# Kernel tuning notes

Measured on AMD Instinct MI355X. Metric: run time of the kernel, lower is better.

Reference implementation:

```python
import jax, jax.numpy as jnp
import numpy as np

ALPHA = 0.2        # LeakyReLU negative slope
NEG_INF = -9.0e15  # mask value used by the torch code


def _gat_layer(x, adj_mask, W, a, concat):
    """Dense multi-head GAT layer.
    x: (N, in_f); adj_mask: (N, N) bool; W: (H, in_f, F); a: (H, 2F, 1).
    Math identical to torch: a_input[p,q] = [h[q], h[p]] so
    e[p,q] = leakyrelu(h[q]@a1 + h[p]@a2) with a = [a1; a2].
    """
    F_out = W.shape[-1]
    h = jnp.einsum('nf,hfo->hno', x, W)                  # (H, N, F)
    a1 = a[:, :F_out, 0]                                 # (H, F) -> applied to h_i (column index q)
    a2 = a[:, F_out:, 0]                                 # (H, F) -> applied to h_j (row index p)
    s1 = jnp.einsum('hnf,hf->hn', h, a1)                 # (H, N)
    s2 = jnp.einsum('hnf,hf->hn', h, a2)                 # (H, N)
    e = jax.nn.leaky_relu(s1[:, None, :] + s2[:, :, None], ALPHA)  # (H, N, N), e[h,p,q]
    e = jnp.where(adj_mask[None, :, :], e, NEG_INF)
    att = jax.nn.softmax(e, axis=-1)                     # softmax over q (dim=1 in torch)
    h_prime = jnp.einsum('hpq,hqf->hpf', att, h)         # (H, N, F)
    if concat:
        N = x.shape[0]
        return h_prime.transpose(1, 0, 2).reshape(N, -1)  # head-order concat, (N, H*F)
    return h_prime.mean(axis=0)                           # (N, F)


def setup_inputs() -> dict:
    key = jax.random.key(0)
    ks = jax.random.split(key, 16)
    N, IN, HID, OUT, H = 2048, 10, 64, 3, 4

    def w(k, shape, fan_in):
        return (jax.random.normal(k, shape, dtype=jnp.float32) * (1.0 / np.sqrt(fan_in))).astype(jnp.float32)

    return {
        'node_features': jax.random.normal(ks[0], (N, IN), dtype=jnp.float32),
        'adj_matrix': jax.random.randint(ks[1], (N, N), 0, 2).astype(jnp.int32),
        'enc_W1': w(ks[2], (IN, HID), IN), 'enc_b1': jnp.zeros((HID,), jnp.float32),
        'enc_W2': w(ks[3], (HID, HID), HID), 'enc_b2': jnp.zeros((HID,), jnp.float32),
        'gat_W0': w(ks[4], (H, HID, HID), HID), 'gat_a0': w(ks[5], (H, 2 * HID, 1), 2 * HID),
        'gat_W1': w(ks[6], (H, HID * H, HID), HID * H), 'gat_a1': w(ks[7], (H, 2 * HID, 1), 2 * HID),
        'gat_W2': w(ks[8], (H, HID * H, OUT), HID * H), 'gat_a2': w(ks[9], (H, 2 * OUT, 1), 2 * OUT),
        'cls_W1': w(ks[10], (OUT, 32), OUT), 'cls_b1': jnp.zeros((32,), jnp.float32),
        'cls_W2': w(ks[11], (32, 1), 32), 'cls_b2': jnp.zeros((1,), jnp.float32),
    }


def reference(node_features, adj_matrix, enc_W1, enc_b1, enc_W2, enc_b2,
              gat_W0, gat_a0, gat_W1, gat_a1, gat_W2, gat_a2,
              cls_W1, cls_b1, cls_W2, cls_b2):
    adj = adj_matrix > 0
    # feature encoder (dropout = identity in eval)
    x = jax.nn.relu(node_features @ enc_W1 + enc_b1) @ enc_W2 + enc_b2
    # GAT stack with ELU between layers
    x = jax.nn.elu(_gat_layer(x, adj, gat_W0, gat_a0, concat=True))
    x = jax.nn.elu(_gat_layer(x, adj, gat_W1, gat_a1, concat=True))
    emb = jax.nn.elu(_gat_layer(x, adj, gat_W2, gat_a2, concat=False))  # (N, OUT)
    # edge classifier: |emb[q] - emb[p]| -> MLP -> sigmoid, (N, N)
    diff = jnp.abs(emb[None, :, :] - emb[:, None, :])                   # (N, N, OUT)
    hidden = jax.nn.relu(diff @ cls_W1 + cls_b1)                        # (N, N, 32)
    edge_probs = jax.nn.sigmoid((hidden @ cls_W2 + cls_b2)[..., 0])     # (N, N)
    return emb, edge_probs
```

## Files before the change

kernel.cpp:

```cpp
#include <hip/hip_runtime.h>
#include <hip/hip_bf16.h>
#include <hip/hip_fp16.h>

#define ALPHA 0.2f
#define LOG2E 1.44269504088896340736f
constexpr int N = 2048;
constexpr int NW = N / 64;

typedef __attribute__((ext_vector_type(8))) short short8v;
typedef __attribute__((ext_vector_type(4))) float f32x4;

__device__ inline unsigned short bf16_rne(float f) {
  unsigned u = __float_as_uint(f);
  return (unsigned short)((u + 0x7fffu + ((u >> 16) & 1u)) >> 16);
}

__device__ inline __half2 relu_h2(__half2 a) {
  unsigned ua = *(unsigned*)&a, ur;
  asm("v_pk_max_f16 %0, %1, 0" : "=v"(ur) : "v"(ua));
  return *(__half2*)&ur;
}


__global__ void __launch_bounds__(512) prep_kernel(
    const float* __restrict__ nf, const int* __restrict__ adj,
    const float* __restrict__ encW1, const float* __restrict__ encb1,
    const float* __restrict__ encW2, const float* __restrict__ encb2,
    const float* __restrict__ gatW0, const float* __restrict__ gatW1,
    unsigned long long* __restrict__ mask,
    unsigned short* __restrict__ wt0hi, unsigned short* __restrict__ wt0lo,
    unsigned short* __restrict__ wt1hi, unsigned short* __restrict__ wt1lo,
    unsigned short* __restrict__ x0hi) {
  const int t = threadIdx.x, b = blockIdx.x;
  {
    int gwave = b * 8 + (t >> 6), lane = t & 63;
#pragma unroll
    for (int i = 0; i < 16; i++) {
      int word = gwave * 16 + i;
      unsigned long long m = __ballot(adj[(size_t)word * 64 + lane] != 0);
      if (lane == 0) mask[word] = m;
    }
  }
  {
    int gtid = b * 512 + t;
    if (gtid < 16384) {
      int head = gtid >> 12, idx = gtid & 4095;
      int o = idx >> 6, k = idx & 63;
      float v = gatW0[(head * 64 + k) * 64 + o];
      unsigned short hb = bf16_rne(v);
      size_t oi = (((((size_t)head * 4 + (o >> 4)) * 2 + (k >> 5)) * 4 + ((k & 31) >> 3)) * 16 + (o & 15)) * 8 + (k & 7);
      wt0hi[oi] = hb;
      wt0lo[oi] = bf16_rne(v - __uint_as_float((unsigned)hb << 16));
    }
    if (gtid < 65536) {
      int head = gtid >> 14, idx = gtid & 16383;
      int o = idx >> 8, k = idx & 255;
      float v = gatW1[((size_t)head * 256 + k) * 64 + o];
      unsigned short hb = bf16_rne(v);
      size_t oi = (((((size_t)head * 4 + (o >> 4)) * 8 + (k >> 5)) * 4 + ((k & 31) >> 3)) * 16 + (o & 15)) * 8 + (k & 7);
      wt1hi[oi] = hb;
      wt1lo[oi] = bf16_rne(v - __uint_as_float((unsigned)hb << 16));
    }
  }
  if (b < 256) {
    __shared__ float nfs[2][4][10], x1e[2][4][64], pred[2][4][4][64];
    const int half = t >> 8, tl = t & 255;
    const int j = tl >> 6, o = tl & 63;
    const int n0 = b * 8 + half * 4;
    if (tl < 40) nfs[half][tl / 10][tl % 10] = nf[n0 * 10 + tl];
    __syncthreads();
    float acc = encb1[o];
#pragma unroll
    for (int k = 0; k < 10; k++) acc = fmaf(nfs[half][j][k], encW1[k * 64 + o], acc);
    x1e[half][j][o] = fmaxf(acc, 0.f);
    __syncthreads();
    {
      const int kq = j;
      float pp0 = 0, pp1 = 0, pp2 = 0, pp3 = 0;
#pragma unroll
      for (int kk = 0; kk < 16; kk++) {
        int k = kq * 16 + kk;
        float wv = encW2[k * 64 + o];
        pp0 = fmaf(x1e[half][0][k], wv, pp0);
        pp1 = fmaf(x1e[half][1][k], wv, pp1);
        pp2 = fmaf(x1e[half][2][k], wv, pp2);
        pp3 = fmaf(x1e[half][3][k], wv, pp3);
      }
      pred[half][kq][0][o] = pp0; pred[half][kq][1][o] = pp1;
      pred[half][kq][2][o] = pp2; pred[half][kq][3][o] = pp3;
    }
    __syncthreads();
    float v = encb2[o] + pred[half][0][j][o] + pred[half][1][j][o] +
              pred[half][2][j][o] + pred[half][3][j][o];
    const int n = n0 + j;
    size_t oi = ((((size_t)(n >> 4) * 2 + (o >> 5)) * 4 + ((o & 31) >> 3)) * 16 + (n & 15)) * 8 + (o & 7);
    x0hi[oi] = bf16_rne(v);
  }
}

template <int K>
__global__ void __launch_bounds__(256, 4)
proj_mfma_kernel(const unsigned short* __restrict__ xhi,
                 const unsigned short* __restrict__ wthi, const unsigned short* __restrict__ wtlo,
                 const float* __restrict__ avec,
                 unsigned short* __restrict__ hT, float* __restrict__ s1, float* __restrict__ s2,
                 float* __restrict__ pm1) {
  constexpr int KS = K / 32;
  const int head = blockIdx.y;
  const int n0 = blockIdx.x * 16;
  const int wave = threadIdx.x >> 6, lane = threadIdx.x & 63;
  const int il = lane & 15, kgrp = lane >> 4;
  const int o0 = wave * 16;
  const unsigned short* __restrict__ Ah = wthi + ((size_t)(head * 4 + wave) * KS) * 512 + lane * 8;
  const unsigned short* __restrict__ Al = wtlo + ((size_t)(head * 4 + wave) * KS) * 512 + lane * 8;
  const unsigned short* __restrict__ Bh = xhi + ((size_t)blockIdx.x * KS) * 512 + lane * 8;
  f32x4 acc = {0, 0, 0, 0};
#pragma unroll
  for (int ks = 0; ks < KS; ks++) {
    short8v ah = *(const short8v*)(Ah + ks * 512);
    short8v al = *(const short8v*)(Al + ks * 512);
    short8v bh = *(const short8v*)(Bh + ks * 512);
    acc = __builtin_amdgcn_mfma_f32_16x16x32_bf16(ah, bh, acc, 0, 0, 0);
    acc = __builtin_amdgcn_mfma_f32_16x16x32_bf16(al, bh, acc, 0, 0, 0);
  }
  const int n = n0 + il;
  const size_t cbase = (((size_t)head * (N / 32) + (n >> 5)) * 4 + wave) * 512;
  const int sub = ((n & 31) >> 3) * 16;
  const int eoff = n & 7;
  float p1 = 0.f, p2 = 0.f;
#pragma unroll
  for (int r = 0; r < 4; r++) {
    const int o = o0 + kgrp * 4 + r;
    hT[cbase + (size_t)(sub + kgrp * 4 + r) * 8 + eoff] = bf16_rne(acc[r]);
    p1 = fmaf(acc[r], avec[head * 128 + o], p1);
    p2 = fmaf(acc[r], avec[head * 128 + 64 + o], p2);
  }
  p1 += __shfl_xor(p1, 16); p1 += __shfl_xor(p1, 32);
  p2 += __shfl_xor(p2, 16); p2 += __shfl_xor(p2, 32);
  __shared__ float s1p[4][16], s2p[4][16];
  if (kgrp == 0) { s1p[wave][il] = p1; s2p[wave][il] = p2; }
  __syncthreads();
  if (threadIdx.x < 16) {
    int nn = n0 + threadIdx.x;
    float v1 = (s1p[0][threadIdx.x] + s1p[1][threadIdx.x] + s1p[2][threadIdx.x] + s1p[3][threadIdx.x]) * LOG2E;
    float v2 = (s2p[0][threadIdx.x] + s2p[1][threadIdx.x] + s2p[2][threadIdx.x] + s2p[3][threadIdx.x]) * LOG2E;
    s1[head * N + nn] = v1;
    s2[head * N + nn] = v2;
    float m1 = v1;
#pragma unroll
    for (int s = 1; s < 16; s <<= 1) m1 = fmaxf(m1, __shfl_xor(m1, s));
    if (threadIdx.x == 0) pm1[head * 128 + blockIdx.x] = m1;
  }
}

template <bool WF32, bool WBF>
__global__ void __launch_bounds__(512, 4)
agg_fused_kernel(const unsigned short* __restrict__ hTu,
                 const float* __restrict__ s1, const float* __restrict__ s2,
                 const float* __restrict__ pm1,
                 const unsigned long long* __restrict__ mask,
                 float* __restrict__ xout, unsigned short* __restrict__ xohi) {
  const int head = blockIdx.y;
  const int p0 = blockIdx.x * 16;
  const int wave = threadIdx.x >> 6, lane = threadIdx.x & 63;
  const int col = lane & 15, kgrp = lane >> 4;
  const int p = p0 + col;
  const float s2pv = s2[head * N + p];
  float sm = fmaxf(pm1[head * 128 + lane], pm1[head * 128 + 64 + lane]);
#pragma unroll
  for (int s = 1; s < 64; s <<= 1) sm = fmaxf(sm, __shfl_xor(sm, s));
  const float mraw = sm + s2pv;
  const float mp = fmaxf(mraw, ALPHA * mraw);
  const float c1 = s2pv - mp;
  const float c2 = ALPHA * s2pv - mp;
  const float* __restrict__ s1h = s1 + head * N;
  const int qbase = wave * 256;
  const unsigned long long* __restrict__ mr = mask + (size_t)p * NW + (qbase >> 6);
  unsigned long long mw0 = mr[0], mw1 = mr[1], mw2 = mr[2], mw3 = mr[3];
  const unsigned short* __restrict__ bbase =
      hTu + (((size_t)head * (N / 32) + wave * 8) * 4) * 512 + lane * 8;

  f32x4 acc[4] = {{0,0,0,0},{0,0,0,0},{0,0,0,0},{0,0,0,0}};
  float wsum = 0.f;
#pragma unroll
  for (int ks = 0; ks < 8; ks++) {
    const int qa = qbase + ks * 32 + kgrp * 8;
    float4 s1v0 = *(const float4*)(s1h + qa);
    float4 s1v1 = *(const float4*)(s1h + qa + 4);
    unsigned long long mwsel = (ks < 2) ? mw0 : (ks < 4) ? mw1 : (ks < 6) ? mw2 : mw3;
    unsigned b8 = (unsigned)((mwsel >> ((ks & 1) * 32 + kgrp * 8)) & 0xFFull);
    float sv[8] = {s1v0.x, s1v0.y, s1v0.z, s1v0.w, s1v1.x, s1v1.y, s1v1.z, s1v1.w};
    float w[8];
#pragma unroll
    for (int e = 0; e < 8; e++) {
      float lr = fmaxf(sv[e] + c1, fmaf(sv[e], ALPHA, c2));
      float ww = exp2f(lr);
      ww = ((b8 >> e) & 1u) ? ww : 0.f;
      wsum += ww;
      w[e] = ww;
    }
    union { short8v s; unsigned u[4]; } av;
#pragma unroll
    for (int e2 = 0; e2 < 4; e2++)
      asm("v_cvt_pk_bf16_f32 %0, %1, %2" : "=v"(av.u[e2]) : "v"(w[2 * e2]), "v"(w[2 * e2 + 1]));
#pragma unroll
    for (int ff = 0; ff < 4; ff++) {
      short8v b_hi = *(const short8v*)(bbase + ((size_t)ks * 4 + ff) * 512);
      acc[ff] = __builtin_amdgcn_mfma_f32_16x16x32_bf16(av.s, b_hi, acc[ff], 0, 0, 0);
    }
  }
  wsum += __shfl_xor(wsum, 16);
  wsum += __shfl_xor(wsum, 32);

  __shared__ float red[8][16][65];
  __shared__ float wred[8][16];
#pragma unroll
  for (int ff = 0; ff < 4; ff++)
#pragma unroll
    for (int r = 0; r < 4; r++)
      red[wave][kgrp * 4 + r][ff * 16 + col] = acc[ff][r];
  if (lane < 16) wred[wave][lane] = wsum;
  __syncthreads();
#pragma unroll
  for (int rep = 0; rep < 2; rep++) {
    int idx = threadIdx.x + rep * 512;
    int pl = idx >> 6, f = idx & 63;
    float num = 0.f, dn = 0.f;
#pragma unroll
    for (int w8 = 0; w8 < 8; w8++) { num += red[w8][pl][f]; dn += wred[w8][pl]; }
    float v = num / dn;
    v = v > 0.f ? v : (__expf(v) - 1.f);
    if (WF32) xout[(size_t)(p0 + pl) * 256 + head * 64 + f] = v;
    if (WBF) {
      size_t oi = ((((size_t)blockIdx.x * 8 + head * 2 + (f >> 5)) * 4 + ((f & 31) >> 3)) * 16 + pl) * 8 + (f & 7);
      xohi[oi] = bf16_rne(v);
    }
  }
}

__global__ void h3_kernel(const float* __restrict__ x, const float* __restrict__ W,
                          const float* __restrict__ a, float* __restrict__ h2,
                          float* __restrict__ s1, float* __restrict__ s2,
                          float* __restrict__ pm1h3) {
  const int n0 = blockIdx.x * 4;
  const int head = threadIdx.x >> 6, o = threadIdx.x & 63;
  __shared__ float xr[4][256];
  for (int k = threadIdx.x; k < 1024; k += 256) xr[k >> 8][k & 255] = x[(size_t)n0 * 256 + k];
  __syncthreads();
  const float* __restrict__ Wh = W + (size_t)head * 256 * 3;
  float m1 = -3.4e38f;
#pragma unroll
  for (int jj = 0; jj < 4; jj++) {
    float a0 = 0.f, a1 = 0.f, a2 = 0.f;
#pragma unroll
    for (int i = 0; i < 4; i++) {
      int k = o + 64 * i;
      float xv = xr[jj][k];
      a0 = fmaf(xv, Wh[k * 3 + 0], a0);
      a1 = fmaf(xv, Wh[k * 3 + 1], a1);
      a2 = fmaf(xv, Wh[k * 3 + 2], a2);
    }
    for (int s = 32; s; s >>= 1) {
      a0 += __shfl_xor(a0, s); a1 += __shfl_xor(a1, s); a2 += __shfl_xor(a2, s);
    }
    float p1 = (a0 * a[head * 6 + 0] + a1 * a[head * 6 + 1] + a2 * a[head * 6 + 2]) * LOG2E;
    float p2 = (a0 * a[head * 6 + 3] + a1 * a[head * 6 + 4] + a2 * a[head * 6 + 5]) * LOG2E;
    m1 = fmaxf(m1, p1);
    if (o == 0) {
      float* hq = h2 + ((size_t)head * N + n0 + jj) * 4;
      hq[0] = a0; hq[1] = a1; hq[2] = a2; hq[3] = 0.f;
      s1[head * N + n0 + jj] = p1;
      s2[head * N + n0 + jj] = p2;
    }
  }
  if (o == 0) pm1h3[head * 512 + blockIdx.x] = m1;
}

__global__ void agg2_kernel(const float* __restrict__ h2, const float* __restrict__ s1,
                            const float* __restrict__ s2, const float* __restrict__ pm1h3,
                            const unsigned long long* __restrict__ mask,
                            float* __restrict__ emb) {
  const int p = blockIdx.x;
  const int head = threadIdx.x >> 6, lane = threadIdx.x & 63;
  const float s2pv = s2[head * N + p];
  float sm = -3.4e38f;
  for (int i = lane; i < 512; i += 64) sm = fmaxf(sm, pm1h3[head * 512 + i]);
#pragma unroll
  for (int s = 1; s < 64; s <<= 1) sm = fmaxf(sm, __shfl_xor(sm, s));
  float mraw = sm + s2pv;
  const float mhv = fmaxf(mraw, ALPHA * mraw);
  const float c1 = s2pv - mhv;
  const float c2 = ALPHA * s2pv - mhv;
  const float* __restrict__ s1h = s1 + head * N;
  float a0 = 0.f, a1 = 0.f, a2 = 0.f, wsum = 0.f;
#pragma unroll 2
  for (int i = 0; i < 32; i++) {
    unsigned long long mwd = mask[(size_t)p * NW + i];
    int q = i * 64 + lane;
    if ((mwd >> lane) & 1ull) {
      float sv = s1h[q];
      float lr = fmaxf(sv + c1, fmaf(sv, ALPHA, c2));
      float w = exp2f(lr);
      float4 hv = *(const float4*)(h2 + ((size_t)head * N + q) * 4);
      a0 = fmaf(w, hv.x, a0);
      a1 = fmaf(w, hv.y, a1);
      a2 = fmaf(w, hv.z, a2);
      wsum += w;
    }
  }
  for (int s = 32; s; s >>= 1) {
    a0 += __shfl_xor(a0, s); a1 += __shfl_xor(a1, s);
    a2 += __shfl_xor(a2, s); wsum += __shfl_xor(wsum, s);
  }
  __shared__ float red[4][4];
  if (lane == 0) { red[head][0] = a0; red[head][1] = a1; red[head][2] = a2; red[head][3] = wsum; }
  __syncthreads();
  if (threadIdx.x < 3) {
    int f = threadIdx.x;
    float v = 0.f;
#pragma unroll
    for (int hh = 0; hh < 4; hh++) v += red[hh][f] / red[hh][3];
    v *= 0.25f;
    v = v > 0.f ? v : (__expf(v) - 1.f);
    emb[p * 3 + f] = v;
  }
}

__global__ void cls_kernel(const float* __restrict__ emb,
                           const float* __restrict__ W1, const float* __restrict__ b1,
                           const float* __restrict__ W2, const float* __restrict__ b2,
                           float* __restrict__ out) {
  int q = blockIdx.x * 256 + threadIdx.x;
  int p0 = blockIdx.y * 8;
  __shared__ float ep[8][3];
  __shared__ __half2 w1h[96], b1h[32], w2h[32];
  __shared__ float b2s;
  int t = threadIdx.x;
  if (t < 96) w1h[t] = __float2half2_rn(W1[t]);
  else if (t < 128) b1h[t - 96] = __float2half2_rn(b1[t - 96]);
  else if (t < 160) w2h[t - 128] = __float2half2_rn(W2[t - 128]);
  else if (t == 160) b2s = b2[0];
  else if (t >= 192 && t < 216) ((float*)ep)[t - 192] = emb[p0 * 3 + t - 192];
  __syncthreads();
  float e0 = emb[q * 3 + 0], e1 = emb[q * 3 + 1], e2 = emb[q * 3 + 2];
  __half2 d0[4], d1[4], d2[4];
#pragma unroll
  for (int ip = 0; ip < 4; ip++) {
    d0[ip] = __floats2half2_rn(fabsf(ep[2 * ip][0] - e0), fabsf(ep[2 * ip + 1][0] - e0));
    d1[ip] = __floats2half2_rn(fabsf(ep[2 * ip][1] - e1), fabsf(ep[2 * ip + 1][1] - e1));
    d2[ip] = __floats2half2_rn(fabsf(ep[2 * ip][2] - e2), fabsf(ep[2 * ip + 1][2] - e2));
  }
  const __half2 hz = __float2half2_rn(0.f);
  __half2 acc[4] = {hz, hz, hz, hz};
#pragma unroll
  for (int j = 0; j < 32; j++) {
    __half2 c0 = w1h[j], c1 = w1h[32 + j], c2 = w1h[64 + j], bb = b1h[j], w2 = w2h[j];
#pragma unroll
    for (int ip = 0; ip < 4; ip++) {
      __half2 hv = __hfma2(d0[ip], c0, __hfma2(d1[ip], c1, __hfma2(d2[ip], c2, bb)));
      hv = relu_h2(hv);
      acc[ip] = __hfma2(hv, w2, acc[ip]);
    }
  }
#pragma unroll
  for (int ip = 0; ip < 4; ip++) {
    float x0 = __low2float(acc[ip]) + b2s;
    float x1 = __high2float(acc[ip]) + b2s;
    out[(size_t)(p0 + 2 * ip) * N + q] = 1.f / (1.f + __expf(-x0));
    out[(size_t)(p0 + 2 * ip + 1) * N + q] = 1.f / (1.f + __expf(-x1));
  }
}

extern "C" void kernel_launch(void* const* d_in, const int* in_sizes, int n_in,
                              void* d_out, int out_size, void* d_ws, size_t ws_size,
                              hipStream_t stream) {
  const float* nf    = (const float*)d_in[0];
  const int*   adj   = (const int*)d_in[1];
  const float* encW1 = (const float*)d_in[2];
  const float* encb1 = (const float*)d_in[3];
  const float* encW2 = (const float*)d_in[4];
  const float* encb2 = (const float*)d_in[5];
  const float* gatW0 = (const float*)d_in[6];
  const float* gata0 = (const float*)d_in[7];
  const float* gatW1 = (const float*)d_in[8];
  const float* gata1 = (const float*)d_in[9];
  const float* gatW2 = (const float*)d_in[10];
  const float* gata2 = (const float*)d_in[11];
  const float* clsW1 = (const float*)d_in[12];
  const float* clsb1 = (const float*)d_in[13];
  const float* clsW2 = (const float*)d_in[14];
  const float* clsb2 = (const float*)d_in[15];

  float* ws = (float*)d_ws;
  unsigned short* hT   = (unsigned short*)ws;
  float* s1   = ws + 262144;
  float* s2   = s1 + 8192;
  float* pm1  = s2 + 8192;
  float* pm1h3= pm1 + 512;
  unsigned short* x0hi = (unsigned short*)(pm1h3 + 2048);
  unsigned short* wt0hi= x0hi + 131072;
  unsigned short* wt0lo= wt0hi + 16384;
  unsigned short* wt1hi= wt0lo + 16384;
  unsigned short* wt1lo= wt1hi + 65536;
  unsigned short* xAhi = wt1lo + 65536;
  float* xB   = (float*)(xAhi + 524288);
  float* h2   = xB + 524288;
  unsigned long long* mask = (unsigned long long*)(h2 + 32768);

  float* emb = (float*)d_out;
  float* eprob = emb + N * 3;

  prep_kernel<<<dim3(512), dim3(512), 0, stream>>>(
      nf, adj, encW1, encb1, encW2, encb2, gatW0, gatW1,
      mask, wt0hi, wt0lo, wt1hi, wt1lo, x0hi);

  proj_mfma_kernel<64><<<dim3(N / 16, 4), dim3(256), 0, stream>>>(
      x0hi, wt0hi, wt0lo, gata0, hT, s1, s2, pm1);
  agg_fused_kernel<false, true><<<dim3(N / 16, 4), dim3(512), 0, stream>>>(
      hT, s1, s2, pm1, mask, nullptr, xAhi);

  proj_mfma_kernel<256><<<dim3(N / 16, 4), dim3(256), 0, stream>>>(
      xAhi, wt1hi, wt1lo, gata1, hT, s1, s2, pm1);
  agg_fused_kernel<true, false><<<dim3(N / 16, 4), dim3(512), 0, stream>>>(
      hT, s1, s2, pm1, mask, xB, nullptr);

  h3_kernel<<<dim3(N / 4), dim3(256), 0, stream>>>(xB, gatW2, gata2, h2, s1, s2, pm1h3);
  agg2_kernel<<<dim3(N), dim3(256), 0, stream>>>(h2, s1, s2, pm1h3, mask, emb);

  cls_kernel<<<dim3(8, N / 8), dim3(256), 0, stream>>>(emb, clsW1, clsb1, clsW2, clsb2, eprob);
}
```

Baseline: 84.88 us.

## Fuse feature encoder and layer-0 weight conversion into first projection kernel

Moves the encoder MLP and the gatW0 bf16 hi/lo split out of prep_kernel into a new proj0_fused_kernel. That kernel computes the encoder output for its 16 nodes in shared memory and runs the layer-0 MFMA projection directly, so the x0hi and wt0 intermediate buffers are no longer written to and read back from global memory. In exchange, each of the 512 blocks recomputes the encoder for its nodes across all 4 heads and converts weights to bf16 on the fly. It also uses large shared arrays and several __syncthreads inside the loop, which can lower occupancy.

```diff
diff --git a/kernel.cpp b/kernel.cpp
--- a/kernel.cpp
+++ b/kernel.cpp
@@ -23,14 +23,9 @@
 
 
 __global__ void __launch_bounds__(512) prep_kernel(
-    const float* __restrict__ nf, const int* __restrict__ adj,
-    const float* __restrict__ encW1, const float* __restrict__ encb1,
-    const float* __restrict__ encW2, const float* __restrict__ encb2,
-    const float* __restrict__ gatW0, const float* __restrict__ gatW1,
+    const int* __restrict__ adj, const float* __restrict__ gatW1,
     unsigned long long* __restrict__ mask,
-    unsigned short* __restrict__ wt0hi, unsigned short* __restrict__ wt0lo,
-    unsigned short* __restrict__ wt1hi, unsigned short* __restrict__ wt1lo,
-    unsigned short* __restrict__ x0hi) {
+    unsigned short* __restrict__ wt1hi, unsigned short* __restrict__ wt1lo) {
   const int t = threadIdx.x, b = blockIdx.x;
   {
     int gwave = b * 8 + (t >> 6), lane = t & 63;
@@ -43,15 +38,6 @@
   }
   {
     int gtid = b * 512 + t;
-    if (gtid < 16384) {
-      int head = gtid >> 12, idx = gtid & 4095;
-      int o = idx >> 6, k = idx & 63;
-      float v = gatW0[(head * 64 + k) * 64 + o];
-      unsigned short hb = bf16_rne(v);
-      size_t oi = (((((size_t)head * 4 + (o >> 4)) * 2 + (k >> 5)) * 4 + ((k & 31) >> 3)) * 16 + (o & 15)) * 8 + (k & 7);
-      wt0hi[oi] = hb;
-      wt0lo[oi] = bf16_rne(v - __uint_as_float((unsigned)hb << 16));
-    }
     if (gtid < 65536) {
       int head = gtid >> 14, idx = gtid & 16383;
       int o = idx >> 8, k = idx & 255;
@@ -62,17 +48,34 @@
       wt1lo[oi] = bf16_rne(v - __uint_as_float((unsigned)hb << 16));
     }
   }
-  if (b < 256) {
-    __shared__ float nfs[2][4][10], x1e[2][4][64], pred[2][4][4][64];
-    const int half = t >> 8, tl = t & 255;
-    const int j = tl >> 6, o = tl & 63;
-    const int n0 = b * 8 + half * 4;
-    if (tl < 40) nfs[half][tl / 10][tl % 10] = nf[n0 * 10 + tl];
-    __syncthreads();
+}
+
+__global__ void __launch_bounds__(256, 4)
+proj0_fused_kernel(const float* __restrict__ nf,
+                   const float* __restrict__ encW1, const float* __restrict__ encb1,
+                   const float* __restrict__ encW2, const float* __restrict__ encb2,
+                   const float* __restrict__ gatW0, const float* __restrict__ avec,
+                   unsigned short* __restrict__ hT, float* __restrict__ s1, float* __restrict__ s2,
+                   float* __restrict__ pm1) {
+  const int head = blockIdx.y;
+  const int n0 = blockIdx.x * 16;
+  const int t = threadIdx.x;
+  __shared__ float nfs[16][10];
+  __shared__ float x1s[4][65];
+  __shared__ float preds[4][4][64];
+  __shared__ float xs[16][65];
+  __shared__ float ws0[64][65];
+  for (int idx = t; idx < 4096; idx += 256) {
+    ws0[idx >> 6][idx & 63] = gatW0[(size_t)head * 4096 + idx];
+  }
+  if (t < 160) nfs[t / 10][t % 10] = nf[(size_t)n0 * 10 + t];
+  __syncthreads();
+  const int j = t >> 6, o = t & 63;
+  for (int batch = 0; batch < 4; batch++) {
     float acc = encb1[o];
 #pragma unroll
-    for (int k = 0; k < 10; k++) acc = fmaf(nfs[half][j][k], encW1[k * 64 + o], acc);
-    x1e[half][j][o] = fmaxf(acc, 0.f);
+    for (int k = 0; k < 10; k++) acc = fmaf(nfs[batch * 4 + j][k], encW1[k * 64 + o], acc);
+    x1s[j][o] = fmaxf(acc, 0.f);
     __syncthreads();
     {
       const int kq = j;
@@ -81,31 +84,75 @@
       for (int kk = 0; kk < 16; kk++) {
         int k = kq * 16 + kk;
         float wv = encW2[k * 64 + o];
-        pp0 = fmaf(x1e[half][0][k], wv, pp0);
-        pp1 = fmaf(x1e[half][1][k], wv, pp1);
-        pp2 = fmaf(x1e[half][2][k], wv, pp2);
-        pp3 = fmaf(x1e[half][3][k], wv, pp3);
+        pp0 = fmaf(x1s[0][k], wv, pp0);
+        pp1 = fmaf(x1s[1][k], wv, pp1);
+        pp2 = fmaf(x1s[2][k], wv, pp2);
+        pp3 = fmaf(x1s[3][k], wv, pp3);
       }
-      pred[half][kq][0][o] = pp0; pred[half][kq][1][o] = pp1;
-      pred[half][kq][2][o] = pp2; pred[half][kq][3][o] = pp3;
+      preds[kq][0][o] = pp0; preds[kq][1][o] = pp1;
+      preds[kq][2][o] = pp2; preds[kq][3][o] = pp3;
     }
     __syncthreads();
-    float v = encb2[o] + pred[half][0][j][o] + pred[half][1][j][o] +
-              pred[half][2][j][o] + pred[half][3][j][o];
-    const int n = n0 + j;
-    size_t oi = ((((size_t)(n >> 4) * 2 + (o >> 5)) * 4 + ((o & 31) >> 3)) * 16 + (n & 15)) * 8 + (o & 7);
-    x0hi[oi] = bf16_rne(v);
-  }
-}
-
-template <int K>
+    xs[batch * 4 + j][o] = encb2[o] + preds[0][j][o] + preds[1][j][o] +
+                           preds[2][j][o] + preds[3][j][o];
+    __syncthreads();
+  }
+  const int wave = t >> 6, lane = t & 63;
+  const int il = lane & 15, kgrp = lane >> 4;
+  const int o0 = wave * 16;
+  f32x4 acc = {0, 0, 0, 0};
+#pragma unroll
+  for (int ks = 0; ks < 2; ks++) {
+    const int kbase = ks * 32 + kgrp * 8;
+    short8v ah, al, bh;
+#pragma unroll
+    for (int e = 0; e < 8; e++) {
+      float wv = ws0[kbase + e][o0 + il];
+      unsigned short hb = bf16_rne(wv);
+      ah[e] = (short)hb;
+      al[e] = (short)bf16_rne(wv - __uint_as_float((unsigned)hb << 16));
+      bh[e] = (short)bf16_rne(xs[il][kbase + e]);
+    }
+    acc = __builtin_amdgcn_mfma_f32_16x16x32_bf16(ah, bh, acc, 0, 0, 0);
+    acc = __builtin_amdgcn_mfma_f32_16x16x32_bf16(al, bh, acc, 0, 0, 0);
+  }
+  const int n = n0 + il;
+  const size_t cbase = (((size_t)head * (N / 32) + (n >> 5)) * 4 + wave) * 512;
+  const int sub = ((n & 31) >> 3) * 16;
+  const int eoff = n & 7;
+  float p1 = 0.f, p2 = 0.f;
+#pragma unroll
+  for (int r = 0; r < 4; r++) {
+    const int oo = o0 + kgrp * 4 + r;
+    hT[cbase + (size_t)(sub + kgrp * 4 + r) * 8 + eoff] = bf16_rne(acc[r]);
+    p1 = fmaf(acc[r], avec[head * 128 + oo], p1);
+    p2 = fmaf(acc[r], avec[head * 128 + 64 + oo], p2);
+  }
+  p1 += __shfl_xor(p1, 16); p1 += __shfl_xor(p1, 32);
+  p2 += __shfl_xor(p2, 16); p2 += __shfl_xor(p2, 32);
+  __shared__ float s1p[4][16], s2p[4][16];
+  if (kgrp == 0) { s1p[wave][il] = p1; s2p[wave][il] = p2; }
+  __syncthreads();
+  if (t < 16) {
+    int nn = n0 + t;
+    float v1 = (s1p[0][t] + s1p[1][t] + s1p[2][t] + s1p[3][t]) * LOG2E;
+    float v2 = (s2p[0][t] + s2p[1][t] + s2p[2][t] + s2p[3][t]) * LOG2E;
+    s1[head * N + nn] = v1;
+    s2[head * N + nn] = v2;
+    float m1 = v1;
+#pragma unroll
+    for (int s = 1; s < 16; s <<= 1) m1 = fmaxf(m1, __shfl_xor(m1, s));
+    if (t == 0) pm1[head * 128 + blockIdx.x] = m1;
+  }
+}
+
 __global__ void __launch_bounds__(256, 4)
 proj_mfma_kernel(const unsigned short* __restrict__ xhi,
                  const unsigned short* __restrict__ wthi, const unsigned short* __restrict__ wtlo,
                  const float* __restrict__ avec,
                  unsigned short* __restrict__ hT, float* __restrict__ s1, float* __restrict__ s2,
                  float* __restrict__ pm1) {
-  constexpr int KS = K / 32;
+  constexpr int KS = 8;
   const int head = blockIdx.y;
   const int n0 = blockIdx.x * 16;
   const int wave = threadIdx.x >> 6, lane = threadIdx.x & 63;
@@ -397,10 +444,7 @@
   float* s2   = s1 + 8192;
   float* pm1  = s2 + 8192;
   float* pm1h3= pm1 + 512;
-  unsigned short* x0hi = (unsigned short*)(pm1h3 + 2048);
-  unsigned short* wt0hi= x0hi + 131072;
-  unsigned short* wt0lo= wt0hi + 16384;
-  unsigned short* wt1hi= wt0lo + 16384;
+  unsigned short* wt1hi= (unsigned short*)(pm1h3 + 2048);
   unsigned short* wt1lo= wt1hi + 65536;
   unsigned short* xAhi = wt1lo + 65536;
   float* xB   = (float*)(xAhi + 524288);
@@ -410,16 +454,14 @@
   float* emb = (float*)d_out;
   float* eprob = emb + N * 3;
 
-  prep_kernel<<<dim3(512), dim3(512), 0, stream>>>(
-      nf, adj, encW1, encb1, encW2, encb2, gatW0, gatW1,
-      mask, wt0hi, wt0lo, wt1hi, wt1lo, x0hi);
-
-  proj_mfma_kernel<64><<<dim3(N / 16, 4), dim3(256), 0, stream>>>(
-      x0hi, wt0hi, wt0lo, gata0, hT, s1, s2, pm1);
+  prep_kernel<<<dim3(512), dim3(512), 0, stream>>>(adj, gatW1, mask, wt1hi, wt1lo);
+
+  proj0_fused_kernel<<<dim3(N / 16, 4), dim3(256), 0, stream>>>(
+      nf, encW1, encb1, encW2, encb2, gatW0, gata0, hT, s1, s2, pm1);
   agg_fused_kernel<false, true><<<dim3(N / 16, 4), dim3(512), 0, stream>>>(
       hT, s1, s2, pm1, mask, nullptr, xAhi);
 
-  proj_mfma_kernel<256><<<dim3(N / 16, 4), dim3(256), 0, stream>>>(
+  proj_mfma_kernel<<<dim3(N / 16, 4), dim3(256), 0, stream>>>(
       xAhi, wt1hi, wt1lo, gata1, hT, s1, s2, pm1);
   agg_fused_kernel<true, false><<<dim3(N / 16, 4), dim3(512), 0, stream>>>(
       hT, s1, s2, pm1, mask, xB, nullptr);
```

Measured after the change: 89.13 us. 5.0% more time.

## Exploit symmetry of edge classifier to compute only upper-triangular tiles

Applied to the files above, without the earlier changes.

The edge MLP output depends on |emb[q]-emb[p]|, which is symmetric, so the classifier now computes only the upper-triangular 64x64 tiles (528 blocks). Each tile is staged in shared memory and written to both (p,q) and its transposed (q,p) location. This roughly halves the MLP arithmetic while keeping the full N×N output write. The cost is a shared-memory tile, extra barriers, a serial loop that maps each block index to a triangular tile, and a transposed write out of the shared tile.

```diff
diff --git a/kernel.cpp b/kernel.cpp
--- a/kernel.cpp
+++ b/kernel.cpp
@@ -326,48 +326,75 @@
   }
 }
 
-__global__ void cls_kernel(const float* __restrict__ emb,
-                           const float* __restrict__ W1, const float* __restrict__ b1,
-                           const float* __restrict__ W2, const float* __restrict__ b2,
-                           float* __restrict__ out) {
-  int q = blockIdx.x * 256 + threadIdx.x;
-  int p0 = blockIdx.y * 8;
-  __shared__ float ep[8][3];
+__global__ void __launch_bounds__(256) cls_kernel(
+    const float* __restrict__ emb,
+    const float* __restrict__ W1, const float* __restrict__ b1,
+    const float* __restrict__ W2, const float* __restrict__ b2,
+    float* __restrict__ out) {
+  int bb = blockIdx.x;
+  int pi = 0, cum = 0;
+  while (cum + (32 - pi) <= bb) { cum += 32 - pi; pi++; }
+  const int qi = pi + (bb - cum);
+  const int P0 = pi * 64, Q0 = qi * 64;
+  const int t = threadIdx.x;
   __shared__ __half2 w1h[96], b1h[32], w2h[32];
   __shared__ float b2s;
-  int t = threadIdx.x;
+  __shared__ float epl[64][3];
+  __shared__ float eql[64][3];
+  __shared__ float stile[64][65];
   if (t < 96) w1h[t] = __float2half2_rn(W1[t]);
   else if (t < 128) b1h[t - 96] = __float2half2_rn(b1[t - 96]);
   else if (t < 160) w2h[t - 128] = __float2half2_rn(W2[t - 128]);
   else if (t == 160) b2s = b2[0];
-  else if (t >= 192 && t < 216) ((float*)ep)[t - 192] = emb[p0 * 3 + t - 192];
-  __syncthreads();
-  float e0 = emb[q * 3 + 0], e1 = emb[q * 3 + 1], e2 = emb[q * 3 + 2];
-  __half2 d0[4], d1[4], d2[4];
-#pragma unroll
-  for (int ip = 0; ip < 4; ip++) {
-    d0[ip] = __floats2half2_rn(fabsf(ep[2 * ip][0] - e0), fabsf(ep[2 * ip + 1][0] - e0));
-    d1[ip] = __floats2half2_rn(fabsf(ep[2 * ip][1] - e1), fabsf(ep[2 * ip + 1][1] - e1));
-    d2[ip] = __floats2half2_rn(fabsf(ep[2 * ip][2] - e2), fabsf(ep[2 * ip + 1][2] - e2));
+  if (t < 192) ((float*)epl)[t] = emb[P0 * 3 + t];
+  else if (t < 224) { int i = t - 192; ((float*)eql)[i] = emb[Q0 * 3 + i]; }
+  __syncthreads();
+  if (t < 160) ((float*)eql)[t + 32] = emb[Q0 * 3 + 32 + t];
+  __syncthreads();
+
+  const int tq = t & 63, pg = t >> 6;
+  const int pb = pg * 16;
+  const float e0 = eql[tq][0], e1 = eql[tq][1], e2 = eql[tq][2];
+  __half2 d0[8], d1[8], d2[8];
+#pragma unroll
+  for (int ip = 0; ip < 8; ip++) {
+    d0[ip] = __floats2half2_rn(fabsf(epl[pb + 2 * ip][0] - e0), fabsf(epl[pb + 2 * ip + 1][0] - e0));
+    d1[ip] = __floats2half2_rn(fabsf(epl[pb + 2 * ip][1] - e1), fabsf(epl[pb + 2 * ip + 1][1] - e1));
+    d2[ip] = __floats2half2_rn(fabsf(epl[pb + 2 * ip][2] - e2), fabsf(epl[pb + 2 * ip + 1][2] - e2));
   }
   const __half2 hz = __float2half2_rn(0.f);
-  __half2 acc[4] = {hz, hz, hz, hz};
+  __half2 acc[8] = {hz, hz, hz, hz, hz, hz, hz, hz};
 #pragma unroll
   for (int j = 0; j < 32; j++) {
-    __half2 c0 = w1h[j], c1 = w1h[32 + j], c2 = w1h[64 + j], bb = b1h[j], w2 = w2h[j];
-#pragma unroll
-    for (int ip = 0; ip < 4; ip++) {
-      __half2 hv = __hfma2(d0[ip], c0, __hfma2(d1[ip], c1, __hfma2(d2[ip], c2, bb)));
+    __half2 c0 = w1h[j], c1 = w1h[32 + j], c2 = w1h[64 + j], bbv = b1h[j], w2 = w2h[j];
+#pragma unroll
+    for (int ip = 0; ip < 8; ip++) {
+      __half2 hv = __hfma2(d0[ip], c0, __hfma2(d1[ip], c1, __hfma2(d2[ip], c2, bbv)));
       hv = relu_h2(hv);
       acc[ip] = __hfma2(hv, w2, acc[ip]);
     }
   }
 #pragma unroll
-  for (int ip = 0; ip < 4; ip++) {
+  for (int ip = 0; ip < 8; ip++) {
     float x0 = __low2float(acc[ip]) + b2s;
     float x1 = __high2float(acc[ip]) + b2s;
-    out[(size_t)(p0 + 2 * ip) * N + q] = 1.f / (1.f + __expf(-x0));
-    out[(size_t)(p0 + 2 * ip + 1) * N + q] = 1.f / (1.f + __expf(-x1));
+    stile[pb + 2 * ip][tq] = 1.f / (1.f + __expf(-x0));
+    stile[pb + 2 * ip + 1][tq] = 1.f / (1.f + __expf(-x1));
+  }
+  __syncthreads();
+#pragma unroll
+  for (int pass = 0; pass < 16; pass++) {
+    int idx = t + pass * 256;
+    int pl = idx >> 6, qq = idx & 63;
+    out[(size_t)(P0 + pl) * N + Q0 + qq] = stile[pl][qq];
+  }
+  if (pi != qi) {
+#pragma unroll
+    for (int pass = 0; pass < 16; pass++) {
+      int idx = t + pass * 256;
+      int ql = idx >> 6, pc = idx & 63;
+      out[(size_t)(Q0 + ql) * N + P0 + pc] = stile[pc][ql];
+    }
   }
 }
 
@@ -427,5 +454,5 @@
   h3_kernel<<<dim3(N / 4), dim3(256), 0, stream>>>(xB, gatW2, gata2, h2, s1, s2, pm1h3);
   agg2_kernel<<<dim3(N), dim3(256), 0, stream>>>(h2, s1, s2, pm1h3, mask, emb);
 
-  cls_kernel<<<dim3(8, N / 8), dim3(256), 0, stream>>>(emb, clsW1, clsb1, clsW2, clsb2, eprob);
-}
+  cls_kernel<<<dim3(528), dim3(256), 0, stream>>>(emb, clsW1, clsb1, clsW2, clsb2, eprob);
+}
```

After: 84.43 us. No clear change (-0.5%).
